# Performance work log

Measured on AMD Instinct MI355X. Metric: run time of the kernel, lower is better.

The kernel has to match this reference:

```python
import jax, jax.numpy as jnp
import numpy as np

EMB = 512
HEADS = 8
WINDOW = 128


def setup_inputs() -> dict:
    key = jax.random.key(0)
    ks = jax.random.split(key, 9)
    s = 1.0 / np.sqrt(EMB)
    x = jax.random.normal(ks[0], (2, 4096, EMB), dtype=jnp.float32)
    mk = lambda k: jax.random.uniform(k, (EMB, EMB), jnp.float32, -s, s)
    mb = lambda k: jax.random.uniform(k, (EMB,), jnp.float32, -s, s)
    return {
        "x": x,
        "Wq": mk(ks[1]), "bq": mb(ks[2]),
        "Wk": mk(ks[3]), "bk": mb(ks[4]),
        "Wv": mk(ks[5]), "bv": mb(ks[6]),
        "Wo": mk(ks[7]), "bo": mb(ks[8]),
    }


def _split_heads(y, b, n):
    # [b, n, emb] -> [b, h, n, d]
    return y.reshape(b, n, HEADS, EMB // HEADS).transpose(0, 2, 1, 3)


def reference(x, Wq, bq, Wk, bk, Wv, bv, Wo, bo):
    b, n, _ = x.shape
    q = _split_heads(x @ Wq.T + bq, b, n)
    k = _split_heads(x @ Wk.T + bk, b, n)
    v = _split_heads(x @ Wv.T + bv, b, n)
    energy = jnp.einsum('bhqd,bhkd->bhqk', q, k)  # [b,h,n,n]
    idx = jnp.arange(n)
    # banded mask: disallowed where |i - j| > window (matches torch loop)
    disallow = jnp.abs(idx[:, None] - idx[None, :]) > WINDOW
    fmin = jnp.float32(np.finfo(np.float32).min)
    energy = jnp.where(disallow[None, None], fmin, energy)
    att = jax.nn.softmax(energy / jnp.float32(np.sqrt(EMB)), axis=-1)
    out = jnp.einsum('bhql,bhld->bhqd', att, v)
    out = out.transpose(0, 2, 1, 3).reshape(b, n, EMB)
    return out @ Wo.T + bo
```

## Files before the change

kernel.cpp:

```cpp
#include <hip/hip_runtime.h>

#define EMB 512
#define HEADS 8
#define HD 64
#define NSEQ 4096
#define BATCH 2
#define WINDOW 128

typedef unsigned short u16;
typedef __attribute__((ext_vector_type(8))) short bf16x8;
typedef __attribute__((ext_vector_type(4))) float f32x4;

#define XS 4194304u
#define WS 262144u
#define BS 512u

__device__ __forceinline__ float bf2f(u16 u) {
    union { unsigned int i; float f; } x;
    x.i = ((unsigned int)u) << 16;
    return x.f;
}

__device__ __forceinline__ u16 f2bf(float f) {
    union { float f; unsigned int i; } x;
    x.f = f;
    unsigned int i = x.i;
    unsigned int lsb = (i >> 16) & 1u;
    i += 0x7fffu + lsb;
    return (u16)(i >> 16);
}

struct raw8 { uint4 lo, hi; };

__device__ __forceinline__ raw8 loadraw8(const void* base, size_t off, int isbf) {
    raw8 r;
    if (isbf) {
        r.lo = *(const uint4*)((const u16*)base + off);
    } else {
        const float* f = (const float*)base + off;
        r.lo = *(const uint4*)f;
        r.hi = *(const uint4*)(f + 4);
    }
    return r;
}

__device__ __forceinline__ uint4 cvt8(const raw8& r, int isbf) {
    if (isbf) return r.lo;
    const float* a = (const float*)&r.lo;
    const float* b = (const float*)&r.hi;
    uint4 o;
    o.x = (unsigned)f2bf(a[0]) | ((unsigned)f2bf(a[1]) << 16);
    o.y = (unsigned)f2bf(a[2]) | ((unsigned)f2bf(a[3]) << 16);
    o.z = (unsigned)f2bf(b[0]) | ((unsigned)f2bf(b[1]) << 16);
    o.w = (unsigned)f2bf(b[2]) | ((unsigned)f2bf(b[3]) << 16);
    return o;
}

__device__ __forceinline__ int probe_bf16(const void* p) {
    const int lane = threadIdx.x & 63;
    u16 w = ((const u16*)p)[lane * 2];
    int e = (w >> 7) & 0xff;
    bool sane = (w == 0) || (e >= 100 && e <= 140);
    unsigned long long m = __ballot(sane);
    return __popcll(m) >= 48;
}

__global__ __launch_bounds__(256)
void prepass(const void* __restrict__ x,
             const void* __restrict__ Wq, const void* __restrict__ bq,
             const void* __restrict__ Wk, const void* __restrict__ bk,
             const void* __restrict__ Wv, const void* __restrict__ bv,
             const void* __restrict__ Wo, const void* __restrict__ bo,
             u16* __restrict__ xb, u16* __restrict__ wb, u16* __restrict__ bb,
             int* __restrict__ flags)
{
    const int fx  = probe_bf16(x);
    const int fwq = probe_bf16(Wq), fbq = probe_bf16(bq);
    const int fwk = probe_bf16(Wk), fbk = probe_bf16(bk);
    const int fwv = probe_bf16(Wv), fbv = probe_bf16(bv);
    const int fwo = probe_bf16(Wo), fbo = probe_bf16(bo);
    if (blockIdx.x == 0 && threadIdx.x == 0) flags[0] = fx;

    size_t idx = ((size_t)blockIdx.x * 256 + threadIdx.x) * 8;
    const size_t T_X = XS, T_W = XS + 4 * (size_t)WS, T_ALL = T_W + 4 * (size_t)BS;
    if (idx >= T_ALL) return;

    const void* src; int fl; u16* dst; size_t off;
    if (idx < T_X) {
        src = x; fl = fx; dst = xb; off = idx;
    } else if (idx < T_W) {
        size_t w = idx - T_X;
        int wi = (int)(w / WS); off = w % WS;
        src = (wi == 0) ? Wq : (wi == 1) ? Wk : (wi == 2) ? Wv : Wo;
        fl  = (wi == 0) ? fwq : (wi == 1) ? fwk : (wi == 2) ? fwv : fwo;
        dst = wb + (size_t)wi * WS;
    } else {
        size_t b = idx - T_W;
        int bi = (int)(b / BS); off = b % BS;
        src = (bi == 0) ? bq : (bi == 1) ? bk : (bi == 2) ? bv : bo;
        fl  = (bi == 0) ? fbq : (bi == 1) ? fbk : (bi == 2) ? fbv : fbo;
        dst = bb + (size_t)bi * BS;
    }
    *(uint4*)(dst + off) = cvt8(loadraw8(src, off, fl), fl);
}

__global__ __launch_bounds__(256)
void qkv_gemm(const u16* __restrict__ X, const u16* __restrict__ Wall,
              const u16* __restrict__ ball,
              u16* __restrict__ qo, u16* __restrict__ ko, u16* __restrict__ vo)
{
    __shared__ __align__(16) u16 As[128 * 32];
    __shared__ __align__(16) u16 Bs[128 * 32];

    const int tid  = threadIdx.x;
    const int wave = tid >> 6;
    const int lane = tid & 63;
    const int quad = lane >> 4;
    const int l16  = lane & 15;
    const int wm = wave >> 1, wn = wave & 1;

    const int m0 = blockIdx.x * 128;
    const int by = blockIdx.y;
    const int wsel = by >> 2;
    const int n0 = (by & 3) * 128;

    const u16* W  = Wall + (size_t)wsel * WS;
    const u16* bi = ball + (size_t)wsel * BS;
    const float oscale = (wsel == 0) ? 0.04419417382415922f : 1.0f;

    const u16* PA = (wsel == 2) ? W : X;
    const u16* PB = (wsel == 2) ? X : W;
    const int abase = (wsel == 2) ? n0 : m0;
    const int bbase = (wsel == 2) ? m0 : n0;

    f32x4 acc[4][4];
#pragma unroll
    for (int i = 0; i < 4; ++i)
#pragma unroll
        for (int j = 0; j < 4; ++j)
            acc[i][j] = (f32x4){0.f, 0.f, 0.f, 0.f};

    const int c1 = tid, c2 = tid + 256;
    const int r1 = c1 >> 2, k1 = (c1 & 3) * 8;
    const int r2 = c2 >> 2, k2 = (c2 & 3) * 8;

    uint4 a1 = *(const uint4*)(PA + (size_t)(abase + r1) * EMB + k1);
    uint4 a2 = *(const uint4*)(PA + (size_t)(abase + r2) * EMB + k2);
    uint4 b1 = *(const uint4*)(PB + (size_t)(bbase + r1) * EMB + k1);
    uint4 b2 = *(const uint4*)(PB + (size_t)(bbase + r2) * EMB + k2);

    for (int kt = 0; kt < 16; ++kt) {
        __syncthreads();
        *(uint4*)&As[c1 * 8] = a1;
        *(uint4*)&As[c2 * 8] = a2;
        *(uint4*)&Bs[c1 * 8] = b1;
        *(uint4*)&Bs[c2 * 8] = b2;
        __syncthreads();

        if (kt < 15) {
            const int kk0 = (kt + 1) * 32;
            a1 = *(const uint4*)(PA + (size_t)(abase + r1) * EMB + kk0 + k1);
            a2 = *(const uint4*)(PA + (size_t)(abase + r2) * EMB + kk0 + k2);
            b1 = *(const uint4*)(PB + (size_t)(bbase + r1) * EMB + kk0 + k1);
            b2 = *(const uint4*)(PB + (size_t)(bbase + r2) * EMB + kk0 + k2);
        }

        bf16x8 af[4], bfr[4];
#pragma unroll
        for (int i = 0; i < 4; ++i)
            af[i] = *(const bf16x8*)&As[(wm * 64 + i * 16 + l16) * 32 + quad * 8];
#pragma unroll
        for (int j = 0; j < 4; ++j)
            bfr[j] = *(const bf16x8*)&Bs[(wn * 64 + j * 16 + l16) * 32 + quad * 8];
#pragma unroll
        for (int i = 0; i < 4; ++i)
#pragma unroll
            for (int j = 0; j < 4; ++j)
                acc[i][j] = __builtin_amdgcn_mfma_f32_16x16x32_bf16(af[i], bfr[j], acc[i][j], 0, 0, 0);
    }

    if (wsel != 2) {
#pragma unroll
        for (int j = 0; j < 4; ++j) {
            const int col = n0 + wn * 64 + j * 16 + l16;
            const float bv_ = bf2f(bi[col]);
            const int h = col >> 6, d = col & 63;
            u16* out = (wsel == 0) ? qo : ko;
#pragma unroll
            for (int i = 0; i < 4; ++i) {
#pragma unroll
                for (int r = 0; r < 4; ++r) {
                    const int row = m0 + wm * 64 + i * 16 + quad * 4 + r;
                    const int b = row >> 12, n = row & 4095;
                    out[(((size_t)(b * HEADS + h) * NSEQ) + n) * HD + d] =
                        f2bf((acc[i][j][r] + bv_) * oscale);
                }
            }
        }
    } else {
#pragma unroll
        for (int i = 0; i < 4; ++i) {
#pragma unroll
            for (int r = 0; r < 4; ++r) {
                const int dglob = n0 + wm * 64 + i * 16 + quad * 4 + r;
                const float bv_ = bf2f(bi[dglob]);
                const int h = dglob >> 6, dd = dglob & 63;
#pragma unroll
                for (int j = 0; j < 4; ++j) {
                    const int ncol = m0 + wn * 64 + j * 16 + l16;
                    const int b = ncol >> 12, n = ncol & 4095;
                    vo[((size_t)(b * HEADS + h) * HD + dd) * NSEQ + n] =
                        f2bf(acc[i][j][r] + bv_);
                }
            }
        }
    }
}

#define KP 72
#define VP 72
__global__ __launch_bounds__(256)
void attn_mfma(const u16* __restrict__ q, const u16* __restrict__ k,
               const u16* __restrict__ vt, u16* __restrict__ ao)
{
    __shared__ __align__(16) u16 Ks[64 * KP];
    __shared__ __align__(16) u16 Vt[80 * VP];
    __shared__ __align__(16) u16 Pb[4][16 * KP];

    const int tid  = threadIdx.x;
    const int wave = tid >> 6;
    const int lane = tid & 63;
    const int quad = lane >> 4;
    const int l16  = lane & 15;

    int wg = blockIdx.y * 64 + blockIdx.x;
    wg = (wg & 7) * 128 + (wg >> 3);
    const int bh = wg >> 6;
    const int q0 = (wg & 63) * 64;

    const int qw = q0 + wave * 16;
    const size_t base = (size_t)bh * NSEQ * HD;
    const bool interior = (q0 >= 128) && (q0 <= NSEQ - 192);

    if (tid < VP) {
        Vt[64 * VP + tid] = (u16)0x3f80;
#pragma unroll
        for (int rr = 65; rr < 80; ++rr) Vt[rr * VP + tid] = 0;
    }

    bf16x8 qa0 = *(const bf16x8*)(q + base + (size_t)(qw + l16) * HD + quad * 8);
    bf16x8 qa1 = *(const bf16x8*)(q + base + (size_t)(qw + l16) * HD + 32 + quad * 8);

    f32x4 O[4], O4;
#pragma unroll
    for (int t = 0; t < 4; ++t) O[t] = (f32x4){0.f, 0.f, 0.f, 0.f};
    O4 = (f32x4){0.f, 0.f, 0.f, 0.f};

    const int key_s[2] = { tid >> 3, (tid + 256) >> 3 };
    const int ch8      = (tid & 7) * 8;

    const int pacol = (quad * 8) ^ ((l16 >> 2) << 4);

    uint4 pkv[2], pvv[2];
#pragma unroll
    for (int s = 0; s < 2; ++s) {
        int kg = q0 - 128 + key_s[s];
        kg = (kg < 0) ? 0 : (kg > NSEQ - 1 ? NSEQ - 1 : kg);
        pkv[s] = *(const uint4*)(k + base + (size_t)kg * HD + ch8);
        int kc = q0 - 128 + ch8;
        kc = (kc < 0) ? 0 : (kc > NSEQ - 8 ? NSEQ - 8 : kc);
        pvv[s] = *(const uint4*)(vt + base + (size_t)key_s[s] * NSEQ + kc);
    }

    for (int c = 0; c < 5; ++c) {
        const int kbase = q0 - 128 + c * 64;

        __syncthreads();
#pragma unroll
        for (int s = 0; s < 2; ++s) {
            *(uint4*)&Ks[key_s[s] * KP + ch8] = pkv[s];
            *(uint4*)&Vt[key_s[s] * VP + ch8] = pvv[s];
        }
        __syncthreads();

        if (c < 4) {
#pragma unroll
            for (int s = 0; s < 2; ++s) {
                int kg = kbase + 64 + key_s[s];
                kg = (kg < 0) ? 0 : (kg > NSEQ - 1 ? NSEQ - 1 : kg);
                pkv[s] = *(const uint4*)(k + base + (size_t)kg * HD + ch8);
                int kc = kbase + 64 + ch8;
                kc = (kc < 0) ? 0 : (kc > NSEQ - 8 ? NSEQ - 8 : kc);
                pvv[s] = *(const uint4*)(vt + base + (size_t)key_s[s] * NSEQ + kc);
            }
        }

        const int gdk = kbase - qw;
        const bool act = (gdk <= 143) && (gdk >= -191) &&
                         (kbase > -64) && (kbase < NSEQ);
        if (act) {
            f32x4 sv[4];
#pragma unroll
            for (int t = 0; t < 4; ++t) {
                const int dk = gdk + t * 16;
                if (dk >= -143 && dk <= 143) {
                    bf16x8 b0 = *(const bf16x8*)&Ks[(t * 16 + l16) * KP + quad * 8];
                    bf16x8 b1 = *(const bf16x8*)&Ks[(t * 16 + l16) * KP + 32 + quad * 8];
                    f32x4 sacc = (f32x4){0.f, 0.f, 0.f, 0.f};
                    sacc = __builtin_amdgcn_mfma_f32_16x16x32_bf16(qa0, b0, sacc, 0, 0, 0);
                    sacc = __builtin_amdgcn_mfma_f32_16x16x32_bf16(qa1, b1, sacc, 0, 0, 0);
                    if (!interior || dk < -113 || dk > 113) {
                        const int jg = kbase + t * 16 + l16;
                        const bool jok = ((unsigned)jg) < (unsigned)NSEQ;
#pragma unroll
                        for (int r = 0; r < 4; ++r) {
                            const int iq = qw + quad * 4 + r;
                            const bool band = ((unsigned)(iq - jg + WINDOW)) <= (unsigned)(2 * WINDOW);
                            if (!(jok && band)) sacc[r] = -1e30f;
                        }
                    }
                    sv[t] = sacc;
                } else {
                    sv[t] = (f32x4){-1e30f, -1e30f, -1e30f, -1e30f};
                }
            }

#pragma unroll
            for (int t = 0; t < 4; ++t) {
                const int tc = (t ^ quad) * 16 + l16;
#pragma unroll
                for (int r = 0; r < 4; ++r) {
                    const float pv = __expf(fminf(sv[t][r], 40.f));
                    Pb[wave][(quad * 4 + r) * KP + tc] = f2bf(pv);
                }
            }

#pragma unroll
            for (int ks2 = 0; ks2 < 2; ++ks2) {
                bf16x8 pa = *(const bf16x8*)&Pb[wave][l16 * KP + (pacol ^ (ks2 * 32))];
#pragma unroll
                for (int t = 0; t < 4; ++t) {
                    bf16x8 vb = *(const bf16x8*)&Vt[(t * 16 + l16) * VP + ks2 * 32 + quad * 8];
                    O[t] = __builtin_amdgcn_mfma_f32_16x16x32_bf16(pa, vb, O[t], 0, 0, 0);
                }
                bf16x8 vb4 = *(const bf16x8*)&Vt[(64 + l16) * VP + ks2 * 32 + quad * 8];
                O4 = __builtin_amdgcn_mfma_f32_16x16x32_bf16(pa, vb4, O4, 0, 0, 0);
            }
        }
    }

    const int bb = bh >> 3, hh = bh & 7;
    float rl[4];
#pragma unroll
    for (int r = 0; r < 4; ++r) {
        const float ls = __shfl(O4[r], lane & 48, 64);
        rl[r] = 1.f / ls;
    }
#pragma unroll
    for (int t = 0; t < 4; ++t)
#pragma unroll
        for (int r = 0; r < 4; ++r) {
            const int iq = qw + quad * 4 + r;
            ao[((size_t)(bb * NSEQ + iq)) * EMB + hh * HD + t * 16 + l16] =
                f2bf(O[t][r] * rl[r]);
        }
}

__global__ __launch_bounds__(256)
void out_gemm(const u16* __restrict__ A, const u16* __restrict__ W,
              const u16* __restrict__ bias, void* __restrict__ out,
              const int* __restrict__ flags)
{
    __shared__ __align__(16) u16 As[128 * 32];
    __shared__ __align__(16) u16 Bs[128 * 32];

    const int tid  = threadIdx.x;
    const int wave = tid >> 6;
    const int lane = tid & 63;
    const int quad = lane >> 4;
    const int l16  = lane & 15;
    const int wm = wave >> 1, wn = wave & 1;

    const int m0 = blockIdx.x * 128;
    const int n0 = blockIdx.y * 128;
    const int fo = flags[0];

    f32x4 acc[4][4];
#pragma unroll
    for (int i = 0; i < 4; ++i)
#pragma unroll
        for (int j = 0; j < 4; ++j)
            acc[i][j] = (f32x4){0.f, 0.f, 0.f, 0.f};

    const int c1 = tid, c2 = tid + 256;
    const int r1 = c1 >> 2, k1 = (c1 & 3) * 8;
    const int r2 = c2 >> 2, k2 = (c2 & 3) * 8;

    uint4 a1 = *(const uint4*)(A + (size_t)(m0 + r1) * EMB + k1);
    uint4 a2 = *(const uint4*)(A + (size_t)(m0 + r2) * EMB + k2);
    uint4 b1 = *(const uint4*)(W + (size_t)(n0 + r1) * EMB + k1);
    uint4 b2 = *(const uint4*)(W + (size_t)(n0 + r2) * EMB + k2);

    for (int kt = 0; kt < 16; ++kt) {
        __syncthreads();
        *(uint4*)&As[c1 * 8] = a1;
        *(uint4*)&As[c2 * 8] = a2;
        *(uint4*)&Bs[c1 * 8] = b1;
        *(uint4*)&Bs[c2 * 8] = b2;
        __syncthreads();

        if (kt < 15) {
            const int kk0 = (kt + 1) * 32;
            a1 = *(const uint4*)(A + (size_t)(m0 + r1) * EMB + kk0 + k1);
            a2 = *(const uint4*)(A + (size_t)(m0 + r2) * EMB + kk0 + k2);
            b1 = *(const uint4*)(W + (size_t)(n0 + r1) * EMB + kk0 + k1);
            b2 = *(const uint4*)(W + (size_t)(n0 + r2) * EMB + kk0 + k2);
        }

        bf16x8 af[4], bfr[4];
#pragma unroll
        for (int i = 0; i < 4; ++i)
            af[i] = *(const bf16x8*)&As[(wm * 64 + i * 16 + l16) * 32 + quad * 8];
#pragma unroll
        for (int j = 0; j < 4; ++j)
            bfr[j] = *(const bf16x8*)&Bs[(wn * 64 + j * 16 + l16) * 32 + quad * 8];
#pragma unroll
        for (int i = 0; i < 4; ++i)
#pragma unroll
            for (int j = 0; j < 4; ++j)
                acc[i][j] = __builtin_amdgcn_mfma_f32_16x16x32_bf16(af[i], bfr[j], acc[i][j], 0, 0, 0);
    }

#pragma unroll
    for (int j = 0; j < 4; ++j) {
        const int col = n0 + wn * 64 + j * 16 + l16;
        const float bv_ = bf2f(bias[col]);
#pragma unroll
        for (int i = 0; i < 4; ++i) {
#pragma unroll
            for (int r = 0; r < 4; ++r) {
                const int row = m0 + wm * 64 + i * 16 + quad * 4 + r;
                const float val = acc[i][j][r] + bv_;
                const size_t idx = (size_t)row * EMB + col;
                if (fo) ((u16*)out)[idx] = f2bf(val);
                else    ((float*)out)[idx] = val;
            }
        }
    }
}

extern "C" void kernel_launch(void* const* d_in, const int* in_sizes, int n_in,
                              void* d_out, int out_size, void* d_ws, size_t ws_size,
                              hipStream_t stream)
{
    const size_t HSZ  = (size_t)BATCH * HEADS * NSEQ * HD;
    char* base = (char*)d_ws;
    int* flags = (int*)base;
    const size_t off = 256;

    u16* xb = (u16*)(base + off);
    u16* wb = xb + XS;
    u16* bb = wb + 4 * (size_t)WS;
    u16* kk = bb + 4 * (size_t)BS;
    u16* vv = kk + HSZ;
    u16* ao = vv + HSZ;
    u16* qq = ao + HSZ;

    const size_t need_t1 = off + 2 * (XS + 4 * (size_t)WS + 4 * (size_t)BS + 4 * HSZ);
    if (ws_size < need_t1) {
        qq = (u16*)d_out;
    }

    prepass<<<dim3(2561), 256, 0, stream>>>(d_in[0], d_in[1], d_in[2], d_in[3],
                                            d_in[4], d_in[5], d_in[6], d_in[7],
                                            d_in[8], xb, wb, bb, flags);
    qkv_gemm<<<dim3(64, 12), 256, 0, stream>>>(xb, wb, bb, qq, kk, vv);
    attn_mfma<<<dim3(64, 16), 256, 0, stream>>>(qq, kk, vv, ao);
    out_gemm<<<dim3(64, 4), 256, 0, stream>>>(ao, wb + 3 * (size_t)WS, bb + 3 * (size_t)BS,
                                              d_out, flags);
}
```

Before: 160.1 us.

## Double-buffer LDS tiles in GEMM and attention kernels to halve barriers

Converts the QKV GEMM, out-projection GEMM and banded attention kernels from single-buffered shared-memory tiles to ping-pong buffers. Each iteration now reads the current buffer while writing the next tile and prefetching two tiles ahead, which removes one of the two barriers per iteration. The ones row used for the softmax denominator moves into its own small buffer. This roughly doubles shared memory per block, which may lower occupancy, and adds register pressure from the deeper prefetch.

```diff
diff --git a/kernel.cpp b/kernel.cpp
--- a/kernel.cpp
+++ b/kernel.cpp
@@ -109,8 +109,8 @@
               const u16* __restrict__ ball,
               u16* __restrict__ qo, u16* __restrict__ ko, u16* __restrict__ vo)
 {
-    __shared__ __align__(16) u16 As[128 * 32];
-    __shared__ __align__(16) u16 Bs[128 * 32];
+    __shared__ __align__(16) u16 As2[2][128 * 32];
+    __shared__ __align__(16) u16 Bs2[2][128 * 32];
 
     const int tid  = threadIdx.x;
     const int wave = tid >> 6;
@@ -148,35 +148,48 @@
     uint4 a2 = *(const uint4*)(PA + (size_t)(abase + r2) * EMB + k2);
     uint4 b1 = *(const uint4*)(PB + (size_t)(bbase + r1) * EMB + k1);
     uint4 b2 = *(const uint4*)(PB + (size_t)(bbase + r2) * EMB + k2);
+    *(uint4*)&As2[0][c1 * 8] = a1;
+    *(uint4*)&As2[0][c2 * 8] = a2;
+    *(uint4*)&Bs2[0][c1 * 8] = b1;
+    *(uint4*)&Bs2[0][c2 * 8] = b2;
+    a1 = *(const uint4*)(PA + (size_t)(abase + r1) * EMB + 32 + k1);
+    a2 = *(const uint4*)(PA + (size_t)(abase + r2) * EMB + 32 + k2);
+    b1 = *(const uint4*)(PB + (size_t)(bbase + r1) * EMB + 32 + k1);
+    b2 = *(const uint4*)(PB + (size_t)(bbase + r2) * EMB + 32 + k2);
+    __syncthreads();
 
     for (int kt = 0; kt < 16; ++kt) {
-        __syncthreads();
-        *(uint4*)&As[c1 * 8] = a1;
-        *(uint4*)&As[c2 * 8] = a2;
-        *(uint4*)&Bs[c1 * 8] = b1;
-        *(uint4*)&Bs[c2 * 8] = b2;
-        __syncthreads();
+        const int cur = kt & 1;
+
+        bf16x8 af[4], bfr[4];
+#pragma unroll
+        for (int i = 0; i < 4; ++i)
+            af[i] = *(const bf16x8*)&As2[cur][(wm * 64 + i * 16 + l16) * 32 + quad * 8];
+#pragma unroll
+        for (int j = 0; j < 4; ++j)
+            bfr[j] = *(const bf16x8*)&Bs2[cur][(wn * 64 + j * 16 + l16) * 32 + quad * 8];
 
         if (kt < 15) {
-            const int kk0 = (kt + 1) * 32;
+            *(uint4*)&As2[cur ^ 1][c1 * 8] = a1;
+            *(uint4*)&As2[cur ^ 1][c2 * 8] = a2;
+            *(uint4*)&Bs2[cur ^ 1][c1 * 8] = b1;
+            *(uint4*)&Bs2[cur ^ 1][c2 * 8] = b2;
+        }
+        if (kt < 14) {
+            const int kk0 = (kt + 2) * 32;
             a1 = *(const uint4*)(PA + (size_t)(abase + r1) * EMB + kk0 + k1);
             a2 = *(const uint4*)(PA + (size_t)(abase + r2) * EMB + kk0 + k2);
             b1 = *(const uint4*)(PB + (size_t)(bbase + r1) * EMB + kk0 + k1);
             b2 = *(const uint4*)(PB + (size_t)(bbase + r2) * EMB + kk0 + k2);
         }
 
-        bf16x8 af[4], bfr[4];
-#pragma unroll
-        for (int i = 0; i < 4; ++i)
-            af[i] = *(const bf16x8*)&As[(wm * 64 + i * 16 + l16) * 32 + quad * 8];
-#pragma unroll
-        for (int j = 0; j < 4; ++j)
-            bfr[j] = *(const bf16x8*)&Bs[(wn * 64 + j * 16 + l16) * 32 + quad * 8];
 #pragma unroll
         for (int i = 0; i < 4; ++i)
 #pragma unroll
             for (int j = 0; j < 4; ++j)
                 acc[i][j] = __builtin_amdgcn_mfma_f32_16x16x32_bf16(af[i], bfr[j], acc[i][j], 0, 0, 0);
+
+        if (kt < 15) __syncthreads();
     }
 
     if (wsel != 2) {
@@ -223,8 +236,9 @@
 void attn_mfma(const u16* __restrict__ q, const u16* __restrict__ k,
                const u16* __restrict__ vt, u16* __restrict__ ao)
 {
-    __shared__ __align__(16) u16 Ks[64 * KP];
-    __shared__ __align__(16) u16 Vt[80 * VP];
+    __shared__ __align__(16) u16 Ks2[2][64 * KP];
+    __shared__ __align__(16) u16 Vt2[2][64 * VP];
+    __shared__ __align__(16) u16 Vones[16 * VP];
     __shared__ __align__(16) u16 Pb[4][16 * KP];
 
     const int tid  = threadIdx.x;
@@ -243,9 +257,9 @@
     const bool interior = (q0 >= 128) && (q0 <= NSEQ - 192);
 
     if (tid < VP) {
-        Vt[64 * VP + tid] = (u16)0x3f80;
-#pragma unroll
-        for (int rr = 65; rr < 80; ++rr) Vt[rr * VP + tid] = 0;
+        Vones[tid] = (u16)0x3f80;
+#pragma unroll
+        for (int rr = 1; rr < 16; ++rr) Vones[rr * VP + tid] = 0;
     }
 
     bf16x8 qa0 = *(const bf16x8*)(q + base + (size_t)(qw + l16) * HD + quad * 8);
@@ -271,25 +285,41 @@
         kc = (kc < 0) ? 0 : (kc > NSEQ - 8 ? NSEQ - 8 : kc);
         pvv[s] = *(const uint4*)(vt + base + (size_t)key_s[s] * NSEQ + kc);
     }
+#pragma unroll
+    for (int s = 0; s < 2; ++s) {
+        *(uint4*)&Ks2[0][key_s[s] * KP + ch8] = pkv[s];
+        *(uint4*)&Vt2[0][key_s[s] * VP + ch8] = pvv[s];
+    }
+#pragma unroll
+    for (int s = 0; s < 2; ++s) {
+        int kg = q0 - 64 + key_s[s];
+        kg = (kg < 0) ? 0 : (kg > NSEQ - 1 ? NSEQ - 1 : kg);
+        pkv[s] = *(const uint4*)(k + base + (size_t)kg * HD + ch8);
+        int kc = q0 - 64 + ch8;
+        kc = (kc < 0) ? 0 : (kc > NSEQ - 8 ? NSEQ - 8 : kc);
+        pvv[s] = *(const uint4*)(vt + base + (size_t)key_s[s] * NSEQ + kc);
+    }
+    __syncthreads();
 
     for (int c = 0; c < 5; ++c) {
+        const int cur = c & 1;
         const int kbase = q0 - 128 + c * 64;
 
-        __syncthreads();
-#pragma unroll
-        for (int s = 0; s < 2; ++s) {
-            *(uint4*)&Ks[key_s[s] * KP + ch8] = pkv[s];
-            *(uint4*)&Vt[key_s[s] * VP + ch8] = pvv[s];
-        }
-        __syncthreads();
-
         if (c < 4) {
 #pragma unroll
             for (int s = 0; s < 2; ++s) {
-                int kg = kbase + 64 + key_s[s];
+                *(uint4*)&Ks2[cur ^ 1][key_s[s] * KP + ch8] = pkv[s];
+                *(uint4*)&Vt2[cur ^ 1][key_s[s] * VP + ch8] = pvv[s];
+            }
+        }
+        if (c < 3) {
+            const int nb = kbase + 128;
+#pragma unroll
+            for (int s = 0; s < 2; ++s) {
+                int kg = nb + key_s[s];
                 kg = (kg < 0) ? 0 : (kg > NSEQ - 1 ? NSEQ - 1 : kg);
                 pkv[s] = *(const uint4*)(k + base + (size_t)kg * HD + ch8);
-                int kc = kbase + 64 + ch8;
+                int kc = nb + ch8;
                 kc = (kc < 0) ? 0 : (kc > NSEQ - 8 ? NSEQ - 8 : kc);
                 pvv[s] = *(const uint4*)(vt + base + (size_t)key_s[s] * NSEQ + kc);
             }
@@ -304,8 +334,8 @@
             for (int t = 0; t < 4; ++t) {
                 const int dk = gdk + t * 16;
                 if (dk >= -143 && dk <= 143) {
-                    bf16x8 b0 = *(const bf16x8*)&Ks[(t * 16 + l16) * KP + quad * 8];
-                    bf16x8 b1 = *(const bf16x8*)&Ks[(t * 16 + l16) * KP + 32 + quad * 8];
+                    bf16x8 b0 = *(const bf16x8*)&Ks2[cur][(t * 16 + l16) * KP + quad * 8];
+                    bf16x8 b1 = *(const bf16x8*)&Ks2[cur][(t * 16 + l16) * KP + 32 + quad * 8];
                     f32x4 sacc = (f32x4){0.f, 0.f, 0.f, 0.f};
                     sacc = __builtin_amdgcn_mfma_f32_16x16x32_bf16(qa0, b0, sacc, 0, 0, 0);
                     sacc = __builtin_amdgcn_mfma_f32_16x16x32_bf16(qa1, b1, sacc, 0, 0, 0);
@@ -340,13 +370,15 @@
                 bf16x8 pa = *(const bf16x8*)&Pb[wave][l16 * KP + (pacol ^ (ks2 * 32))];
 #pragma unroll
                 for (int t = 0; t < 4; ++t) {
-                    bf16x8 vb = *(const bf16x8*)&Vt[(t * 16 + l16) * VP + ks2 * 32 + quad * 8];
+                    bf16x8 vb = *(const bf16x8*)&Vt2[cur][(t * 16 + l16) * VP + ks2 * 32 + quad * 8];
                     O[t] = __builtin_amdgcn_mfma_f32_16x16x32_bf16(pa, vb, O[t], 0, 0, 0);
                 }
-                bf16x8 vb4 = *(const bf16x8*)&Vt[(64 + l16) * VP + ks2 * 32 + quad * 8];
+                bf16x8 vb4 = *(const bf16x8*)&Vones[l16 * VP + ks2 * 32 + quad * 8];
                 O4 = __builtin_amdgcn_mfma_f32_16x16x32_bf16(pa, vb4, O4, 0, 0, 0);
             }
         }
+
+        if (c < 4) __syncthreads();
     }
 
     const int bb = bh >> 3, hh = bh & 7;
@@ -371,8 +403,8 @@
               const u16* __restrict__ bias, void* __restrict__ out,
               const int* __restrict__ flags)
 {
-    __shared__ __align__(16) u16 As[128 * 32];
-    __shared__ __align__(16) u16 Bs[128 * 32];
+    __shared__ __align__(16) u16 As2[2][128 * 32];
+    __shared__ __align__(16) u16 Bs2[2][128 * 32];
 
     const int tid  = threadIdx.x;
     const int wave = tid >> 6;
@@ -400,35 +432,48 @@
     uint4 a2 = *(const uint4*)(A + (size_t)(m0 + r2) * EMB + k2);
     uint4 b1 = *(const uint4*)(W + (size_t)(n0 + r1) * EMB + k1);
     uint4 b2 = *(const uint4*)(W + (size_t)(n0 + r2) * EMB + k2);
+    *(uint4*)&As2[0][c1 * 8] = a1;
+    *(uint4*)&As2[0][c2 * 8] = a2;
+    *(uint4*)&Bs2[0][c1 * 8] = b1;
+    *(uint4*)&Bs2[0][c2 * 8] = b2;
+    a1 = *(const uint4*)(A + (size_t)(m0 + r1) * EMB + 32 + k1);
+    a2 = *(const uint4*)(A + (size_t)(m0 + r2) * EMB + 32 + k2);
+    b1 = *(const uint4*)(W + (size_t)(n0 + r1) * EMB + 32 + k1);
+    b2 = *(const uint4*)(W + (size_t)(n0 + r2) * EMB + 32 + k2);
+    __syncthreads();
 
     for (int kt = 0; kt < 16; ++kt) {
-        __syncthreads();
-        *(uint4*)&As[c1 * 8] = a1;
-        *(uint4*)&As[c2 * 8] = a2;
-        *(uint4*)&Bs[c1 * 8] = b1;
-        *(uint4*)&Bs[c2 * 8] = b2;
-        __syncthreads();
+        const int cur = kt & 1;
+
+        bf16x8 af[4], bfr[4];
+#pragma unroll
+        for (int i = 0; i < 4; ++i)
+            af[i] = *(const bf16x8*)&As2[cur][(wm * 64 + i * 16 + l16) * 32 + quad * 8];
+#pragma unroll
+        for (int j = 0; j < 4; ++j)
+            bfr[j] = *(const bf16x8*)&Bs2[cur][(wn * 64 + j * 16 + l16) * 32 + quad * 8];
 
         if (kt < 15) {
-            const int kk0 = (kt + 1) * 32;
+            *(uint4*)&As2[cur ^ 1][c1 * 8] = a1;
+            *(uint4*)&As2[cur ^ 1][c2 * 8] = a2;
+            *(uint4*)&Bs2[cur ^ 1][c1 * 8] = b1;
+            *(uint4*)&Bs2[cur ^ 1][c2 * 8] = b2;
+        }
+        if (kt < 14) {
+            const int kk0 = (kt + 2) * 32;
             a1 = *(const uint4*)(A + (size_t)(m0 + r1) * EMB + kk0 + k1);
             a2 = *(const uint4*)(A + (size_t)(m0 + r2) * EMB + kk0 + k2);
             b1 = *(const uint4*)(W + (size_t)(n0 + r1) * EMB + kk0 + k1);
             b2 = *(const uint4*)(W + (size_t)(n0 + r2) * EMB + kk0 + k2);
         }
 
-        bf16x8 af[4], bfr[4];
-#pragma unroll
-        for (int i = 0; i < 4; ++i)
-            af[i] = *(const bf16x8*)&As[(wm * 64 + i * 16 + l16) * 32 + quad * 8];
-#pragma unroll
-        for (int j = 0; j < 4; ++j)
-            bfr[j] = *(const bf16x8*)&Bs[(wn * 64 + j * 16 + l16) * 32 + quad * 8];
 #pragma unroll
         for (int i = 0; i < 4; ++i)
 #pragma unroll
             for (int j = 0; j < 4; ++j)
                 acc[i][j] = __builtin_amdgcn_mfma_f32_16x16x32_bf16(af[i], bfr[j], acc[i][j], 0, 0, 0);
+
+        if (kt < 15) __syncthreads();
     }
 
 #pragma unroll
```

Measured after the change: 150.1 us. 1.07x faster.
